# Performance work log

Hardware: AMD Instinct MI355X
Metric: run time of the kernel (lower is better)

The kernel has to match this reference:

```python
import jax, jax.numpy as jnp
import numpy as np

B, T, D, H = 8, 4096, 512, 64

def setup_inputs() -> dict:
    key = jax.random.key(0)
    ks = jax.random.split(key, 6)
    s = 0.02  # small init scale so exp(K), exp(wbias) stay numerically tame
    return {
        "x": jax.random.normal(ks[0], (B, T, D), dtype=jnp.float32),
        "wq": jax.random.normal(ks[1], (H, D), dtype=jnp.float32) * s,
        "bq": jnp.zeros((H,), dtype=jnp.float32),
        "wk": jax.random.normal(ks[2], (H, D), dtype=jnp.float32) * s,
        "bk": jnp.zeros((H,), dtype=jnp.float32),
        "wv": jax.random.normal(ks[3], (H, D), dtype=jnp.float32) * s,
        "bv": jnp.zeros((H,), dtype=jnp.float32),
        "wp": jax.random.normal(ks[4], (D, H), dtype=jnp.float32) * s,
        "bp": jnp.zeros((D,), dtype=jnp.float32),
        "wbias": jax.random.normal(ks[5], (T, T), dtype=jnp.float32) * s,
    }

def reference(x, wq, bq, wk, bk, wv, bv, wp, bp, wbias):
    # Q, K, V projections: [B, T, H]
    Q = jnp.einsum('btd,hd->bth', x, wq) + bq
    K = jnp.einsum('btd,hd->bth', x, wk) + bk
    V = jnp.einsum('btd,hd->bth', x, wv) + bv
    ew = jnp.exp(wbias)              # [T, T], computed once
    eK = jnp.exp(K)                  # [B, T, H]
    num = jnp.einsum('ts,bsh->bth', ew, eK * V)
    den = jnp.einsum('ts,bsh->bth', ew, eK)
    Yt = jax.nn.sigmoid(Q) * (num / den)
    # output projection back to dim: [B, T, D]
    return jnp.einsum('bth,dh->btd', Yt, wp) + bp
```

## Files before the change

kernel.cpp:

```cpp
#include <hip/hip_runtime.h>
#include <math.h>

typedef _Float16 f16;
typedef __attribute__((ext_vector_type(8))) _Float16 f16x8;
typedef __attribute__((ext_vector_type(4))) _Float16 f16x4;
typedef __attribute__((ext_vector_type(4))) float f32x4;
typedef __attribute__((ext_vector_type(16))) float f32x16;

#define MFMA16(a, b, c) __builtin_amdgcn_mfma_f32_16x16x32_f16((a), (b), (c), 0, 0, 0)
#define MFMA32(a, b, c) __builtin_amdgcn_mfma_f32_32x32x16_f16((a), (b), (c), 0, 0, 0)

__device__ __forceinline__ void gld16(const f16* g, f16* l) {
  __builtin_amdgcn_global_load_lds(
      (const __attribute__((address_space(1))) unsigned int*)g,
      (__attribute__((address_space(3))) unsigned int*)l, 16, 0, 0);
}

__device__ __forceinline__ f16x8 pack8(const float* src) {
  float4 f0 = *(const float4*)src;
  float4 f1 = *(const float4*)(src + 4);
  f16x8 v;
  v[0] = (f16)f0.x; v[1] = (f16)f0.y; v[2] = (f16)f0.z; v[3] = (f16)f0.w;
  v[4] = (f16)f1.x; v[5] = (f16)f1.y; v[6] = (f16)f1.z; v[7] = (f16)f1.w;
  return v;
}

__global__ __launch_bounds__(256) void prep_ew(const float* __restrict__ wb,
                                               f16* __restrict__ ew) {
  const size_t stride = (size_t)gridDim.x * 256;
  const size_t total = (size_t)4096 * 4096 / 4;
  for (size_t i = (size_t)blockIdx.x * 256 + threadIdx.x; i < total; i += stride) {
    float4 f = ((const float4*)wb)[i];
    f16x4 o;
    o.x = (f16)expf(f.x); o.y = (f16)expf(f.y);
    o.z = (f16)expf(f.z); o.w = (f16)expf(f.w);
    ((f16x4*)ew)[i] = o;
  }
}

__global__ __launch_bounds__(256) void prep_w(const float* __restrict__ wq,
                                              const float* __restrict__ wk,
                                              const float* __restrict__ wv,
                                              const float* __restrict__ wp,
                                              f16* __restrict__ wqkvb,
                                              f16* __restrict__ wpb) {
  int i = blockIdx.x * 256 + threadIdx.x;
  wqkvb[i] = (f16)wk[i];
  wqkvb[32768 + i] = (f16)wv[i];
  wqkvb[65536 + i] = (f16)wq[i];
  wpb[i] = (f16)wp[i];
}

__global__ __launch_bounds__(256) void k1_qkv(const float* __restrict__ x,
                                              const f16* __restrict__ wqkvb,
                                              const float* __restrict__ bq,
                                              const float* __restrict__ bk,
                                              const float* __restrict__ bv,
                                              f16* __restrict__ sigQ,
                                              f16* __restrict__ XT) {
  __shared__ alignas(16) f16 sW[192 * 64];
  __shared__ alignas(16) f16 sX[64 * 64];
  const int tid = threadIdx.x;
  const int wave = tid >> 6, lane = tid & 63;
  const int m0 = blockIdx.x * 64;
  const int l15 = lane & 15;

  f32x4 accQ[4], accK[4], accV[4];
#pragma unroll
  for (int j = 0; j < 4; ++j) {
    accQ[j] = (f32x4){0.f, 0.f, 0.f, 0.f};
    accK[j] = (f32x4){0.f, 0.f, 0.f, 0.f};
    accV[j] = (f32x4){0.f, 0.f, 0.f, 0.f};
  }

  const int sc8 = tid & 7;
  const int wr8 = (tid >> 3) & 7;
  const int wcol = (sc8 ^ wr8) * 8;

  for (int ks = 0; ks < 512; ks += 64) {
#pragma unroll
    for (int q = 0; q < 6; ++q) {
      int r = q * 32 + (tid >> 3);
      gld16(wqkvb + (size_t)r * 512 + ks + wcol, &sW[r * 64 + sc8 * 8]);
    }
#pragma unroll
    for (int u = 0; u < 2; ++u) {
      int un = tid + u * 256;
      int r = un >> 3, c8 = un & 7;
      *(f16x8*)&sX[r * 64 + ((c8 ^ (r & 7)) * 8)] =
          pack8(x + (size_t)(m0 + r) * 512 + ks + c8 * 8);
    }
    __syncthreads();
#pragma unroll
    for (int kk = 0; kk < 2; ++kk) {
      const int c = kk * 4 + (lane >> 4);
      const int rK = wave * 16 + l15;
      const int rV = 64 + rK;
      f16x8 aK = *(const f16x8*)&sW[rK * 64 + ((c ^ (rK & 7)) * 8)];
      f16x8 aV = *(const f16x8*)&sW[rV * 64 + ((c ^ (rV & 7)) * 8)];
      f16x8 aQ = *(const f16x8*)&sX[rK * 64 + ((c ^ (rK & 7)) * 8)];
#pragma unroll
      for (int j = 0; j < 4; ++j) {
        const int rX = j * 16 + l15;
        const int rWq = 128 + j * 16 + l15;
        f16x8 bx = *(const f16x8*)&sX[rX * 64 + ((c ^ (rX & 7)) * 8)];
        f16x8 bw = *(const f16x8*)&sW[rWq * 64 + ((c ^ (rWq & 7)) * 8)];
        accK[j] = MFMA16(aK, bx, accK[j]);
        accV[j] = MFMA16(aV, bx, accV[j]);
        accQ[j] = MFMA16(aQ, bw, accQ[j]);
      }
    }
    __syncthreads();
  }
  const int b = m0 >> 12, t0 = m0 & 4095;
#pragma unroll
  for (int j = 0; j < 4; ++j) {
    const int h = j * 16 + l15;
    const float bqv = bq[h];
#pragma unroll
    for (int r = 0; r < 4; ++r) {
      const int m = m0 + wave * 16 + (lane >> 4) * 4 + r;
      const float v = accQ[j][r] + bqv;
      sigQ[(size_t)m * 64 + h] = (f16)(1.f / (1.f + expf(-v)));
    }
  }
#pragma unroll
  for (int r = 0; r < 4; ++r) {
    const int h = wave * 16 + (lane >> 4) * 4 + r;
    const float bkv = bk[h], bvv = bv[h];
    const size_t rowKV = (size_t)(b * 128 + h) * 4096;
    const size_t rowK = (size_t)(b * 128 + 64 + h) * 4096;
#pragma unroll
    for (int j = 0; j < 4; ++j) {
      const int t = t0 + j * 16 + l15;
      const float ek = expf(accK[j][r] + bkv);
      const float ev = accV[j][r] + bvv;
      XT[rowKV + t] = (f16)(ek * ev);
      XT[rowK + t] = (f16)ek;
    }
  }
}

__global__ __launch_bounds__(512, 2) void k2_big(const f16* __restrict__ A,
                                                 const f16* __restrict__ Bm,
                                                 const f16* __restrict__ sigQ,
                                                 f16* __restrict__ Yt) {
  __shared__ alignas(16) f16 sA[2][128 * 128];
  __shared__ alignas(16) f16 sB[2][128 * 128];
  const int tid = threadIdx.x;
  const int wave = tid >> 6, lane = tid & 63;
  const int kh = wave >> 2;
  const int wq = wave & 3;
  const int wr = wq >> 1, wc = wq & 1;
  const int bid = blockIdx.x;
  const int b = bid & 7;
  const int m0 = (bid >> 3) * 128;
  const f16* Bbase = Bm + (size_t)(b * 128) * 4096;

  const int srow = tid >> 4;
  const int sc16 = tid & 15;
  const int gcol = ((sc16 ^ (srow & 7)) * 8);

  f32x16 acc[2][2];
#pragma unroll
  for (int i = 0; i < 2; ++i)
#pragma unroll
    for (int j = 0; j < 2; ++j)
#pragma unroll
      for (int r = 0; r < 16; ++r) acc[i][j][r] = 0.f;

#define K2_STAGE(buf, ks)                                                              \
  do {                                                                                 \
    _Pragma("unroll") for (int q = 0; q < 4; ++q) {                                    \
      int r = q * 32 + srow;                                                           \
      gld16(A + (size_t)(m0 + r) * 4096 + (ks) + gcol, &sA[buf][r * 128 + sc16 * 8]);  \
      gld16(Bbase + (size_t)r * 4096 + (ks) + gcol, &sB[buf][r * 128 + sc16 * 8]);     \
    }                                                                                  \
  } while (0)

  K2_STAGE(0, 0);
  __syncthreads();
  const int rA0 = wr * 64 + (lane & 31);
  const int rB0 = wc * 32 + (lane & 31);
  const int nk = 4096 / 128;
  for (int t = 0; t < nk; ++t) {
    const int buf = t & 1;
    if (t + 1 < nk) K2_STAGE(buf ^ 1, (t + 1) * 128);
#pragma unroll
    for (int kk = 0; kk < 4; ++kk) {
      const int c = kh * 8 + kk * 2 + (lane >> 5);
      const int cx = (c ^ (rA0 & 7)) * 8;
      f16x8 a0 = *(const f16x8*)&sA[buf][rA0 * 128 + cx];
      f16x8 a1 = *(const f16x8*)&sA[buf][(rA0 + 32) * 128 + cx];
      f16x8 b0 = *(const f16x8*)&sB[buf][rB0 * 128 + cx];
      f16x8 b1 = *(const f16x8*)&sB[buf][(rB0 + 64) * 128 + cx];
      acc[0][0] = MFMA32(a0, b0, acc[0][0]);
      acc[0][1] = MFMA32(a0, b1, acc[0][1]);
      acc[1][0] = MFMA32(a1, b0, acc[1][0]);
      acc[1][1] = MFMA32(a1, b1, acc[1][1]);
    }
    __syncthreads();
  }
#undef K2_STAGE

  float* red = (float*)sA;
  if (kh == 1) {
#pragma unroll
    for (int i = 0; i < 2; ++i)
#pragma unroll
      for (int j = 0; j < 2; ++j)
#pragma unroll
        for (int r = 0; r < 16; ++r)
          red[(((wq * 2 + i) * 2 + j) << 10) + (r << 6) + lane] = acc[i][j][r];
  }
  __syncthreads();
  if (kh == 0) {
#pragma unroll
    for (int i = 0; i < 2; ++i)
#pragma unroll
      for (int j = 0; j < 2; ++j)
#pragma unroll
        for (int r = 0; r < 16; ++r)
          acc[i][j][r] += red[(((wq * 2 + i) * 2 + j) << 10) + (r << 6) + lane];
    const int colh = wc * 32 + (lane & 31);
    const int rbase = (lane >> 5) * 4;
#pragma unroll
    for (int i = 0; i < 2; ++i) {
      const int tb = m0 + wr * 64 + i * 32;
#pragma unroll
      for (int r = 0; r < 16; ++r) {
        const int trow = tb + (r & 3) + 8 * (r >> 2) + rbase;
        const size_t mrow = (size_t)b * 4096 + trow;
        const float num = acc[i][0][r];
        const float den = acc[i][1][r];
        const float sq = (float)sigQ[mrow * 64 + colh];
        Yt[mrow * 64 + colh] = (f16)(sq * num / den);
      }
    }
  }
}

__global__ __launch_bounds__(256) void k4_out(const f16* __restrict__ Yt,
                                              const f16* __restrict__ wpb,
                                              const float* __restrict__ bp,
                                              float* __restrict__ out) {
  __shared__ alignas(16) f16 sA[128 * 64];
  __shared__ alignas(16) f16 sB[128 * 64];
  const int tid = threadIdx.x;
  const int wave = tid >> 6, lane = tid & 63;
  const int m0 = blockIdx.x * 128;
  const int n0 = blockIdx.y * 128;
  const int wm = (wave >> 1) * 64;
  const int wn = (wave & 1) * 64;
  const int l15 = lane & 15;
  const int sc8 = tid & 7;
  const int scol = (sc8 ^ ((tid >> 3) & 7)) * 8;

#pragma unroll
  for (int q = 0; q < 4; ++q) {
    int r = q * 32 + (tid >> 3);
    gld16(Yt + (size_t)(m0 + r) * 64 + scol, &sA[r * 64 + sc8 * 8]);
    gld16(wpb + (size_t)(n0 + r) * 64 + scol, &sB[r * 64 + sc8 * 8]);
  }
  __syncthreads();

  f32x4 acc[4][4];
#pragma unroll
  for (int i = 0; i < 4; ++i)
#pragma unroll
    for (int j = 0; j < 4; ++j) acc[i][j] = (f32x4){0.f, 0.f, 0.f, 0.f};

#pragma unroll
  for (int kk = 0; kk < 2; ++kk) {
    const int c = kk * 4 + (lane >> 4);
    f16x8 af[4], bfr[4];
#pragma unroll
    for (int i = 0; i < 4; ++i) {
      const int r = wm + i * 16 + l15;
      af[i] = *(const f16x8*)&sA[r * 64 + ((c ^ (r & 7)) * 8)];
    }
#pragma unroll
    for (int j = 0; j < 4; ++j) {
      const int r = wn + j * 16 + l15;
      bfr[j] = *(const f16x8*)&sB[r * 64 + ((c ^ (r & 7)) * 8)];
    }
#pragma unroll
    for (int i = 0; i < 4; ++i)
#pragma unroll
      for (int j = 0; j < 4; ++j) acc[i][j] = MFMA16(af[i], bfr[j], acc[i][j]);
  }

#pragma unroll
  for (int i = 0; i < 4; ++i) {
    const int row = m0 + wm + i * 16 + (lane >> 4) * 4;
#pragma unroll
    for (int j = 0; j < 4; ++j) {
      const int col = n0 + wn + j * 16 + l15;
      const float bpv = bp[col];
#pragma unroll
      for (int r = 0; r < 4; ++r)
        out[(size_t)(row + r) * 512 + col] = acc[i][j][r] + bpv;
    }
  }
}

extern "C" void kernel_launch(void* const* d_in, const int* in_sizes, int n_in,
                              void* d_out, int out_size, void* d_ws, size_t ws_size,
                              hipStream_t stream) {
  const float* x = (const float*)d_in[0];
  const float* wq = (const float*)d_in[1];
  const float* bq = (const float*)d_in[2];
  const float* wk = (const float*)d_in[3];
  const float* bk = (const float*)d_in[4];
  const float* wv = (const float*)d_in[5];
  const float* bv = (const float*)d_in[6];
  const float* wp = (const float*)d_in[7];
  const float* bp = (const float*)d_in[8];
  const float* wbias = (const float*)d_in[9];
  float* out = (float*)d_out;

  char* ws = (char*)d_ws;
  f16* ew = (f16*)(ws);
  f16* XT = (f16*)(ws + 33554432);
  f16* sigQ = (f16*)(ws + 41943040);
  f16* Yt = (f16*)(ws + 46137344);
  f16* wqkvb = (f16*)(ws + 50331648);
  f16* wpb = (f16*)(ws + 50528256);

  prep_ew<<<4096, 256, 0, stream>>>(wbias, ew);
  prep_w<<<128, 256, 0, stream>>>(wq, wk, wv, wp, wqkvb, wpb);
  k1_qkv<<<512, 256, 0, stream>>>(x, wqkvb, bq, bk, bv, sigQ, XT);
  k2_big<<<256, 512, 0, stream>>>(ew, XT, sigQ, Yt);
  k4_out<<<dim3(256, 4), 256, 0, stream>>>(Yt, wpb, bp, out);
}
```

Baseline: 117.9 us.

## Deepen k2 prefetch with explicit vmcnt waits, remap blocks, widen LDS swizzle

Restructures the k2_big main loop so two stages are in flight: it issues tile t+2 after a barrier and waits with explicit vmcnt counters instead of a full __syncthreads per iteration. It also remaps block indices so consecutive blocks share the same batch's B operand, which should improve L2 reuse. The LDS XOR swizzle is widened from 8 to 16 columns to reduce bank conflicts. The risks are the hand-written waitcnt/barrier sequencing, and dropping the occupancy hint from launch_bounds.

```diff
diff --git a/kernel.cpp b/kernel.cpp
--- a/kernel.cpp
+++ b/kernel.cpp
@@ -141,10 +141,10 @@
   }
 }
 
-__global__ __launch_bounds__(512, 2) void k2_big(const f16* __restrict__ A,
-                                                 const f16* __restrict__ Bm,
-                                                 const f16* __restrict__ sigQ,
-                                                 f16* __restrict__ Yt) {
+__global__ __launch_bounds__(512) void k2_big(const f16* __restrict__ A,
+                                              const f16* __restrict__ Bm,
+                                              const f16* __restrict__ sigQ,
+                                              f16* __restrict__ Yt) {
   __shared__ alignas(16) f16 sA[2][128 * 128];
   __shared__ alignas(16) f16 sB[2][128 * 128];
   const int tid = threadIdx.x;
@@ -153,13 +153,13 @@
   const int wq = wave & 3;
   const int wr = wq >> 1, wc = wq & 1;
   const int bid = blockIdx.x;
-  const int b = bid & 7;
-  const int m0 = (bid >> 3) * 128;
+  const int b = (bid >> 3) & 7;
+  const int m0 = ((bid & 7) + 8 * (bid >> 6)) * 128;
   const f16* Bbase = Bm + (size_t)(b * 128) * 4096;
 
   const int srow = tid >> 4;
   const int sc16 = tid & 15;
-  const int gcol = ((sc16 ^ (srow & 7)) * 8);
+  const int gcol = (sc16 ^ (srow & 15)) * 8;
 
   f32x16 acc[2][2];
 #pragma unroll
@@ -179,17 +179,21 @@
   } while (0)
 
   K2_STAGE(0, 0);
-  __syncthreads();
+  K2_STAGE(1, 128);
+  asm volatile("s_waitcnt vmcnt(8)" ::: "memory");
+  __builtin_amdgcn_s_barrier();
+  asm volatile("" ::: "memory");
+
   const int rA0 = wr * 64 + (lane & 31);
   const int rB0 = wc * 32 + (lane & 31);
+  const int l15x = lane & 15;
   const int nk = 4096 / 128;
   for (int t = 0; t < nk; ++t) {
     const int buf = t & 1;
-    if (t + 1 < nk) K2_STAGE(buf ^ 1, (t + 1) * 128);
 #pragma unroll
     for (int kk = 0; kk < 4; ++kk) {
       const int c = kh * 8 + kk * 2 + (lane >> 5);
-      const int cx = (c ^ (rA0 & 7)) * 8;
+      const int cx = (c ^ l15x) * 8;
       f16x8 a0 = *(const f16x8*)&sA[buf][rA0 * 128 + cx];
       f16x8 a1 = *(const f16x8*)&sA[buf][(rA0 + 32) * 128 + cx];
       f16x8 b0 = *(const f16x8*)&sB[buf][rB0 * 128 + cx];
@@ -199,10 +203,23 @@
       acc[1][0] = MFMA32(a1, b0, acc[1][0]);
       acc[1][1] = MFMA32(a1, b1, acc[1][1]);
     }
-    __syncthreads();
+    if (t + 1 < nk) {
+      asm volatile("s_waitcnt lgkmcnt(0)" ::: "memory");
+      __builtin_amdgcn_s_barrier();
+      asm volatile("" ::: "memory");
+      if (t + 2 < nk) {
+        K2_STAGE(buf, (t + 2) * 128);
+        asm volatile("s_waitcnt vmcnt(8)" ::: "memory");
+      } else {
+        asm volatile("s_waitcnt vmcnt(0)" ::: "memory");
+      }
+      __builtin_amdgcn_s_barrier();
+      asm volatile("" ::: "memory");
+    }
   }
 #undef K2_STAGE
 
+  __syncthreads();
   float* red = (float*)sA;
   if (kh == 1) {
 #pragma unroll
```

Result: faster. 97.30 us (-17.5%).

## Pre-swizzle operands into MFMA fragment layout, drop LDS staging, fuse output projection

Applied to the files above, without the earlier changes.

Stores exp(wbias), the K/V products and wp in a fragment-major layout so each lane can load its MFMA operand straight from global memory with one 16-byte load. The big GEMM therefore no longer stages tiles through LDS, drops the split-K reduction, and runs 256 threads with higher occupancy. The output projection is fused into its epilogue, and the two prep kernels are merged into one. This removes LDS traffic, barriers, the Yt round trip and two launches. In exchange, global loads are now issued directly without double-buffered prefetch, which risks exposing latency on the 4096-deep K loop.

```diff
diff --git a/kernel.cpp b/kernel.cpp
--- a/kernel.cpp
+++ b/kernel.cpp
@@ -25,30 +25,57 @@
   return v;
 }
 
-__global__ __launch_bounds__(256) void prep_ew(const float* __restrict__ wb,
-                                               f16* __restrict__ ew) {
-  const size_t stride = (size_t)gridDim.x * 256;
-  const size_t total = (size_t)4096 * 4096 / 4;
-  for (size_t i = (size_t)blockIdx.x * 256 + threadIdx.x; i < total; i += stride) {
-    float4 f = ((const float4*)wb)[i];
-    f16x4 o;
-    o.x = (f16)expf(f.x); o.y = (f16)expf(f.y);
-    o.z = (f16)expf(f.z); o.w = (f16)expf(f.w);
-    ((f16x4*)ew)[i] = o;
-  }
-}
-
-__global__ __launch_bounds__(256) void prep_w(const float* __restrict__ wq,
-                                              const float* __restrict__ wk,
-                                              const float* __restrict__ wv,
-                                              const float* __restrict__ wp,
-                                              f16* __restrict__ wqkvb,
-                                              f16* __restrict__ wpb) {
-  int i = blockIdx.x * 256 + threadIdx.x;
-  wqkvb[i] = (f16)wk[i];
-  wqkvb[32768 + i] = (f16)wv[i];
-  wqkvb[65536 + i] = (f16)wq[i];
-  wpb[i] = (f16)wp[i];
+__global__ __launch_bounds__(256) void prep_eww(const float* __restrict__ wb,
+                                                f16* __restrict__ eww,
+                                                const float* __restrict__ wq,
+                                                const float* __restrict__ wk,
+                                                const float* __restrict__ wv,
+                                                const float* __restrict__ wp,
+                                                f16* __restrict__ wqkvb,
+                                                f16* __restrict__ wpf) {
+  __shared__ float sL[32 * 261];
+  const int tid = threadIdx.x;
+  const int bid = blockIdx.x;
+  const int mblk = bid >> 4;
+  const int cg = bid & 15;
+#pragma unroll
+  for (int u = 0; u < 8; ++u) {
+    int d = u * 256 + tid;
+    int row = d >> 6, c4 = d & 63;
+    float4 v = *(const float4*)(wb + (size_t)(mblk * 32 + row) * 4096 + cg * 256 + c4 * 4);
+    float* p = &sL[row * 261 + c4 * 4];
+    p[0] = v.x; p[1] = v.y; p[2] = v.z; p[3] = v.w;
+  }
+  __syncthreads();
+  const int wv_ = tid >> 6, lane = tid & 63;
+  const int row = lane & 31, kh = (lane >> 5) * 8;
+#pragma unroll
+  for (int q = 0; q < 4; ++q) {
+    const int cl = wv_ * 4 + q;
+    const float* src = &sL[row * 261 + cl * 16 + kh];
+    f16x8 o;
+#pragma unroll
+    for (int e = 0; e < 8; ++e) o[e] = (f16)expf(src[e]);
+    *(f16x8*)(eww + ((((size_t)mblk * 256) + cg * 16 + cl) * 64 + lane) * 8) = o;
+  }
+  if (bid < 128) {
+    int i = bid * 256 + tid;
+    wqkvb[i] = (f16)wk[i];
+    wqkvb[32768 + i] = (f16)wv[i];
+    wqkvb[65536 + i] = (f16)wq[i];
+  }
+  if (bid == 128) {
+#pragma unroll
+    for (int u = 0; u < 16; ++u) {
+      int d = u * 256 + tid;
+      int dcb = d >> 8, c = (d >> 6) & 3, l = d & 63;
+      const float* src = wp + (size_t)(dcb * 32 + (l & 31)) * 64 + c * 16 + (l >> 5) * 8;
+      f16x8 o;
+#pragma unroll
+      for (int e = 0; e < 8; ++e) o[e] = (f16)src[e];
+      *(f16x8*)(wpf + ((size_t)d << 3)) = o;
+    }
+  }
 }
 
 __global__ __launch_bounds__(256) void k1_qkv(const float* __restrict__ x,
@@ -57,7 +84,7 @@
                                               const float* __restrict__ bk,
                                               const float* __restrict__ bv,
                                               f16* __restrict__ sigQ,
-                                              f16* __restrict__ XT) {
+                                              f16* __restrict__ XT2) {
   __shared__ alignas(16) f16 sW[192 * 64];
   __shared__ alignas(16) f16 sX[64 * 64];
   const int tid = threadIdx.x;
@@ -124,42 +151,51 @@
       sigQ[(size_t)m * 64 + h] = (f16)(1.f / (1.f + expf(-v)));
     }
   }
+  f16* sT = sW;
 #pragma unroll
   for (int r = 0; r < 4; ++r) {
     const int h = wave * 16 + (lane >> 4) * 4 + r;
     const float bkv = bk[h], bvv = bv[h];
-    const size_t rowKV = (size_t)(b * 128 + h) * 4096;
-    const size_t rowK = (size_t)(b * 128 + 64 + h) * 4096;
 #pragma unroll
     for (int j = 0; j < 4; ++j) {
-      const int t = t0 + j * 16 + l15;
+      const int tl = j * 16 + l15;
       const float ek = expf(accK[j][r] + bkv);
       const float ev = accV[j][r] + bvv;
-      XT[rowKV + t] = (f16)(ek * ev);
-      XT[rowK + t] = (f16)ek;
-    }
-  }
-}
-
-__global__ __launch_bounds__(512, 2) void k2_big(const f16* __restrict__ A,
-                                                 const f16* __restrict__ Bm,
+      sT[h * 72 + tl] = (f16)(ek * ev);
+      sT[(64 + h) * 72 + tl] = (f16)ek;
+    }
+  }
+  __syncthreads();
+  const int cb = wave;
+  const int l31 = lane & 31;
+  const int khalf = (lane >> 5) * 8;
+#pragma unroll
+  for (int cl = 0; cl < 4; ++cl) {
+    f16x8 v = *(const f16x8*)&sT[(cb * 32 + l31) * 72 + cl * 16 + khalf];
+    *(f16x8*)(XT2 + ((((size_t)b * 4 + cb) * 256 + (t0 >> 4) + cl) * 64 + lane) * 8) = v;
+  }
+}
+
+__global__ __launch_bounds__(256, 4) void k2_big(const f16* __restrict__ eww,
+                                                 const f16* __restrict__ XT2,
                                                  const f16* __restrict__ sigQ,
-                                                 f16* __restrict__ Yt) {
-  __shared__ alignas(16) f16 sA[2][128 * 128];
-  __shared__ alignas(16) f16 sB[2][128 * 128];
+                                                 const f16* __restrict__ wpf,
+                                                 const float* __restrict__ bp,
+                                                 float* __restrict__ out) {
+  __shared__ alignas(16) f16 sYt[128 * 72];
   const int tid = threadIdx.x;
-  const int wave = tid >> 6, lane = tid & 63;
-  const int kh = wave >> 2;
-  const int wq = wave & 3;
-  const int wr = wq >> 1, wc = wq & 1;
+  const int w = tid >> 6, lane = tid & 63;
+  const int l31 = lane & 31, lhi = lane >> 5;
   const int bid = blockIdx.x;
-  const int b = bid & 7;
-  const int m0 = (bid >> 3) * 128;
-  const f16* Bbase = Bm + (size_t)(b * 128) * 4096;
-
-  const int srow = tid >> 4;
-  const int sc16 = tid & 15;
-  const int gcol = ((sc16 ^ (srow & 7)) * 8);
+  const int mt = (bid & 7) * 4 + (bid >> 6);
+  const int b = (bid >> 3) & 7;
+  const int m0 = mt * 128;
+
+  const f16* pa0 = eww + ((size_t)(mt * 4 + (w >> 1) * 2) * 256 * 64 + lane) * 8;
+  const f16* pa1 = pa0 + (size_t)256 * 512;
+  const int cbn = w & 1;
+  const f16* pbn = XT2 + ((size_t)(b * 4 + cbn) * 256 * 64 + lane) * 8;
+  const f16* pbd = XT2 + ((size_t)(b * 4 + 2 + cbn) * 256 * 64 + lane) * 8;
 
   f32x16 acc[2][2];
 #pragma unroll
@@ -169,137 +205,51 @@
 #pragma unroll
       for (int r = 0; r < 16; ++r) acc[i][j][r] = 0.f;
 
-#define K2_STAGE(buf, ks)                                                              \
-  do {                                                                                 \
-    _Pragma("unroll") for (int q = 0; q < 4; ++q) {                                    \
-      int r = q * 32 + srow;                                                           \
-      gld16(A + (size_t)(m0 + r) * 4096 + (ks) + gcol, &sA[buf][r * 128 + sc16 * 8]);  \
-      gld16(Bbase + (size_t)r * 4096 + (ks) + gcol, &sB[buf][r * 128 + sc16 * 8]);     \
-    }                                                                                  \
-  } while (0)
-
-  K2_STAGE(0, 0);
+#pragma unroll 4
+  for (int c = 0; c < 256; ++c) {
+    f16x8 a0 = *(const f16x8*)(pa0 + (size_t)c * 512);
+    f16x8 a1 = *(const f16x8*)(pa1 + (size_t)c * 512);
+    f16x8 bn = *(const f16x8*)(pbn + (size_t)c * 512);
+    f16x8 bd = *(const f16x8*)(pbd + (size_t)c * 512);
+    acc[0][0] = MFMA32(a0, bn, acc[0][0]);
+    acc[0][1] = MFMA32(a0, bd, acc[0][1]);
+    acc[1][0] = MFMA32(a1, bn, acc[1][0]);
+    acc[1][1] = MFMA32(a1, bd, acc[1][1]);
+  }
+
+  const int wm = (w >> 1) * 64;
+  const int hcol = cbn * 32 + l31;
+#pragma unroll
+  for (int i = 0; i < 2; ++i) {
+#pragma unroll
+    for (int r = 0; r < 16; ++r) {
+      const int row = wm + i * 32 + (r & 3) + 8 * (r >> 2) + 4 * lhi;
+      const float sq = (float)sigQ[((size_t)b * 4096 + m0 + row) * 64 + hcol];
+      sYt[row * 72 + hcol] = (f16)(sq * acc[i][0][r] / acc[i][1][r]);
+    }
+  }
   __syncthreads();
-  const int rA0 = wr * 64 + (lane & 31);
-  const int rB0 = wc * 32 + (lane & 31);
-  const int nk = 4096 / 128;
-  for (int t = 0; t < nk; ++t) {
-    const int buf = t & 1;
-    if (t + 1 < nk) K2_STAGE(buf ^ 1, (t + 1) * 128);
-#pragma unroll
-    for (int kk = 0; kk < 4; ++kk) {
-      const int c = kh * 8 + kk * 2 + (lane >> 5);
-      const int cx = (c ^ (rA0 & 7)) * 8;
-      f16x8 a0 = *(const f16x8*)&sA[buf][rA0 * 128 + cx];
-      f16x8 a1 = *(const f16x8*)&sA[buf][(rA0 + 32) * 128 + cx];
-      f16x8 b0 = *(const f16x8*)&sB[buf][rB0 * 128 + cx];
-      f16x8 b1 = *(const f16x8*)&sB[buf][(rB0 + 64) * 128 + cx];
-      acc[0][0] = MFMA32(a0, b0, acc[0][0]);
-      acc[0][1] = MFMA32(a0, b1, acc[0][1]);
-      acc[1][0] = MFMA32(a1, b0, acc[1][0]);
-      acc[1][1] = MFMA32(a1, b1, acc[1][1]);
-    }
-    __syncthreads();
-  }
-#undef K2_STAGE
-
-  float* red = (float*)sA;
-  if (kh == 1) {
-#pragma unroll
-    for (int i = 0; i < 2; ++i)
-#pragma unroll
-      for (int j = 0; j < 2; ++j)
-#pragma unroll
-        for (int r = 0; r < 16; ++r)
-          red[(((wq * 2 + i) * 2 + j) << 10) + (r << 6) + lane] = acc[i][j][r];
-  }
-  __syncthreads();
-  if (kh == 0) {
-#pragma unroll
-    for (int i = 0; i < 2; ++i)
-#pragma unroll
-      for (int j = 0; j < 2; ++j)
-#pragma unroll
-        for (int r = 0; r < 16; ++r)
-          acc[i][j][r] += red[(((wq * 2 + i) * 2 + j) << 10) + (r << 6) + lane];
-    const int colh = wc * 32 + (lane & 31);
-    const int rbase = (lane >> 5) * 4;
-#pragma unroll
-    for (int i = 0; i < 2; ++i) {
-      const int tb = m0 + wr * 64 + i * 32;
-#pragma unroll
-      for (int r = 0; r < 16; ++r) {
-        const int trow = tb + (r & 3) + 8 * (r >> 2) + rbase;
-        const size_t mrow = (size_t)b * 4096 + trow;
-        const float num = acc[i][0][r];
-        const float den = acc[i][1][r];
-        const float sq = (float)sigQ[mrow * 64 + colh];
-        Yt[mrow * 64 + colh] = (f16)(sq * num / den);
-      }
-    }
-  }
-}
-
-__global__ __launch_bounds__(256) void k4_out(const f16* __restrict__ Yt,
-                                              const f16* __restrict__ wpb,
-                                              const float* __restrict__ bp,
-                                              float* __restrict__ out) {
-  __shared__ alignas(16) f16 sA[128 * 64];
-  __shared__ alignas(16) f16 sB[128 * 64];
-  const int tid = threadIdx.x;
-  const int wave = tid >> 6, lane = tid & 63;
-  const int m0 = blockIdx.x * 128;
-  const int n0 = blockIdx.y * 128;
-  const int wm = (wave >> 1) * 64;
-  const int wn = (wave & 1) * 64;
-  const int l15 = lane & 15;
-  const int sc8 = tid & 7;
-  const int scol = (sc8 ^ ((tid >> 3) & 7)) * 8;
-
-#pragma unroll
-  for (int q = 0; q < 4; ++q) {
-    int r = q * 32 + (tid >> 3);
-    gld16(Yt + (size_t)(m0 + r) * 64 + scol, &sA[r * 64 + sc8 * 8]);
-    gld16(wpb + (size_t)(n0 + r) * 64 + scol, &sB[r * 64 + sc8 * 8]);
-  }
-  __syncthreads();
-
-  f32x4 acc[4][4];
-#pragma unroll
-  for (int i = 0; i < 4; ++i)
-#pragma unroll
-    for (int j = 0; j < 4; ++j) acc[i][j] = (f32x4){0.f, 0.f, 0.f, 0.f};
-
-#pragma unroll
-  for (int kk = 0; kk < 2; ++kk) {
-    const int c = kk * 4 + (lane >> 4);
-    f16x8 af[4], bfr[4];
-#pragma unroll
-    for (int i = 0; i < 4; ++i) {
-      const int r = wm + i * 16 + l15;
-      af[i] = *(const f16x8*)&sA[r * 64 + ((c ^ (r & 7)) * 8)];
-    }
-#pragma unroll
-    for (int j = 0; j < 4; ++j) {
-      const int r = wn + j * 16 + l15;
-      bfr[j] = *(const f16x8*)&sB[r * 64 + ((c ^ (r & 7)) * 8)];
-    }
-#pragma unroll
-    for (int i = 0; i < 4; ++i)
-#pragma unroll
-      for (int j = 0; j < 4; ++j) acc[i][j] = MFMA16(af[i], bfr[j], acc[i][j]);
-  }
-
-#pragma unroll
-  for (int i = 0; i < 4; ++i) {
-    const int row = m0 + wm + i * 16 + (lane >> 4) * 4;
-#pragma unroll
-    for (int j = 0; j < 4; ++j) {
-      const int col = n0 + wn + j * 16 + l15;
-      const float bpv = bp[col];
-#pragma unroll
-      for (int r = 0; r < 4; ++r)
-        out[(size_t)(row + r) * 512 + col] = acc[i][j][r] + bpv;
+
+  f16x8 ay[4];
+#pragma unroll
+  for (int c = 0; c < 4; ++c)
+    ay[c] = *(const f16x8*)&sYt[(w * 32 + l31) * 72 + c * 16 + lhi * 8];
+#pragma unroll
+  for (int cbo = 0; cbo < 16; ++cbo) {
+    f32x16 oacc;
+#pragma unroll
+    for (int r = 0; r < 16; ++r) oacc[r] = 0.f;
+#pragma unroll
+    for (int c = 0; c < 4; ++c) {
+      f16x8 bw = *(const f16x8*)(wpf + (((size_t)cbo * 4 + c) * 64 + lane) * 8);
+      oacc = MFMA32(ay[c], bw, oacc);
+    }
+    const int od = cbo * 32 + l31;
+    const float bpv = bp[od];
+#pragma unroll
+    for (int r = 0; r < 16; ++r) {
+      const int orow = w * 32 + (r & 3) + 8 * (r >> 2) + 4 * lhi;
+      out[((size_t)(b * 4096 + m0 + orow)) * 512 + od] = oacc[r] + bpv;
     }
   }
 }
@@ -320,16 +270,13 @@
   float* out = (float*)d_out;
 
   char* ws = (char*)d_ws;
-  f16* ew = (f16*)(ws);
-  f16* XT = (f16*)(ws + 33554432);
+  f16* eww = (f16*)(ws);
+  f16* XT2 = (f16*)(ws + 33554432);
   f16* sigQ = (f16*)(ws + 41943040);
-  f16* Yt = (f16*)(ws + 46137344);
-  f16* wqkvb = (f16*)(ws + 50331648);
-  f16* wpb = (f16*)(ws + 50528256);
-
-  prep_ew<<<4096, 256, 0, stream>>>(wbias, ew);
-  prep_w<<<128, 256, 0, stream>>>(wq, wk, wv, wp, wqkvb, wpb);
-  k1_qkv<<<512, 256, 0, stream>>>(x, wqkvb, bq, bk, bv, sigQ, XT);
-  k2_big<<<256, 512, 0, stream>>>(ew, XT, sigQ, Yt);
-  k4_out<<<dim3(256, 4), 256, 0, stream>>>(Yt, wpb, bp, out);
-}
+  f16* wqkvb = (f16*)(ws + 46137344);
+  f16* wpf = (f16*)(ws + 46333952);
+
+  prep_eww<<<2048, 256, 0, stream>>>(wbias, eww, wq, wk, wv, wp, wqkvb, wpf);
+  k1_qkv<<<512, 256, 0, stream>>>(x, wqkvb, bq, bk, bv, sigQ, XT2);
+  k2_big<<<256, 256, 0, stream>>>(eww, XT2, sigQ, wpf, bp, out);
+}
```

Result: slower. 142.6 us (+20.9%).
